# Performance work log

Hardware: AMD Instinct MI355X
Metric: run time of the kernel (lower is better)

Reference implementation:

```python
import jax, jax.numpy as jnp
import numpy as np

NEG_SLOPE = 0.2


def gat_layer(x, src, dst, W, a_src, a_dst, b, heads, out_c, concat):
    N = x.shape[0]
    h = (x @ W).reshape(N, heads, out_c)                      # [N,H,C]
    alpha_s = jnp.einsum('nhc,hc->nh', h, a_src)              # [N,H]
    alpha_d = jnp.einsum('nhc,hc->nh', h, a_dst)              # [N,H]
    e = jax.nn.leaky_relu(alpha_s[src] + alpha_d[dst], NEG_SLOPE)  # [E,H]
    # softmax over incoming edges per destination node (segment softmax)
    m = jax.ops.segment_max(e, dst, num_segments=N)
    m = jnp.where(jnp.isfinite(m), m, 0.0)
    ex = jnp.exp(e - m[dst])
    denom = jax.ops.segment_sum(ex, dst, num_segments=N)
    alpha = ex / (denom[dst] + 1e-16)                         # [E,H]
    out = jax.ops.segment_sum(alpha[:, :, None] * h[src], dst, num_segments=N)  # [N,H,C]
    out = out.reshape(N, heads * out_c) if concat else out.mean(axis=1)
    return out + b


def setup_inputs() -> dict:
    key = jax.random.key(0)
    ks = jax.random.split(key, 12)
    N, E, D, H, C, G = 20000, 160000, 256, 4, 128, 64
    x = jax.random.normal(ks[0], (N, D), dtype=jnp.float32)
    edge_index = jax.random.randint(ks[1], (2, E), 0, N)
    batch = jnp.sort(jax.random.randint(ks[2], (N,), 0, G))
    s = 0.05
    params = {
        'W1': jax.random.normal(ks[3], (D, H * C), jnp.float32) * s,
        'a_src1': jax.random.normal(ks[4], (H, C), jnp.float32) * s,
        'a_dst1': jax.random.normal(ks[5], (H, C), jnp.float32) * s,
        'b1': jnp.zeros((H * C,), jnp.float32),
        'W2': jax.random.normal(ks[6], (H * C, C), jnp.float32) * s,
        'a_src2': jax.random.normal(ks[7], (1, C), jnp.float32) * s,
        'a_dst2': jax.random.normal(ks[8], (1, C), jnp.float32) * s,
        'b2': jnp.zeros((C,), jnp.float32),
        'fc1_W': jax.random.normal(ks[9], (C, C // 2), jnp.float32) * s,
        'fc1_b': jnp.zeros((C // 2,), jnp.float32),
        'fc2_W': jax.random.normal(ks[10], (C // 2, 1), jnp.float32) * s,
        'fc2_b': jnp.zeros((1,), jnp.float32),
    }
    return dict(x=x, edge_index=edge_index, batch=batch, **params)


def reference(x, edge_index, batch, W1, a_src1, a_dst1, b1, W2, a_src2, a_dst2, b2,
              fc1_W, fc1_b, fc2_W, fc2_b):
    N = x.shape[0]
    G = 64  # number of graphs
    # add self-loops (PyG GATConv default)
    loop = jnp.arange(N, dtype=edge_index.dtype)
    src = jnp.concatenate([edge_index[0], loop])
    dst = jnp.concatenate([edge_index[1], loop])
    h = jax.nn.relu(gat_layer(x, src, dst, W1, a_src1, a_dst1, b1, 4, 128, True))
    h = gat_layer(h, src, dst, W2, a_src2, a_dst2, b2, 1, 128, False)
    # global mean pool per graph
    sums = jax.ops.segment_sum(h, batch, num_segments=G)
    cnts = jax.ops.segment_sum(jnp.ones((N,), h.dtype), batch, num_segments=G)
    pooled = sums / jnp.maximum(cnts, 1.0)[:, None]          # [G,128]
    out = jax.nn.relu(pooled @ fc1_W + fc1_b)
    return out @ fc2_W + fc2_b                                # [G,1]
```

## Files before the change

kernel.cpp:

```cpp
#include <hip/hip_runtime.h>
#include <hip/hip_bf16.h>
#include <cstdint>
#include <cstddef>

#define NEG_SLOPE 0.2f

typedef __attribute__((ext_vector_type(8))) __bf16 bf16x8;
typedef __attribute__((ext_vector_type(4))) __bf16 bf16x4;
typedef __attribute__((ext_vector_type(2))) __bf16 bf16x2;
typedef __attribute__((ext_vector_type(4))) float  f32x4;

template<int MF, int NF, bool STORE_BF16>
__global__ __launch_bounds__(256) void gemm_mfma(
    const __bf16* __restrict__ A, const __bf16* __restrict__ Bt,
    void* __restrict__ Cout, int M, int N, int K)
{
    const int tid  = threadIdx.x;
    const int wave = tid >> 6, lane = tid & 63;
    const int wr = wave >> 1, wc = wave & 1;
    const int rowbase = blockIdx.y * (32 * MF) + wr * (16 * MF);
    const int colbase = blockIdx.x * (32 * NF) + wc * (16 * NF);
    const int l15 = lane & 15, kg = lane >> 4;

    size_t aoff[MF], boff[NF];
    #pragma unroll
    for (int mf = 0; mf < MF; ++mf) {
        int r = rowbase + mf * 16 + l15;
        if (r > M - 1) r = M - 1;
        aoff[mf] = (size_t)r * K + kg * 8;
    }
    #pragma unroll
    for (int nf = 0; nf < NF; ++nf) {
        int c = colbase + nf * 16 + l15;
        boff[nf] = (size_t)c * K + kg * 8;
    }

    f32x4 acc[MF][NF];
    #pragma unroll
    for (int mf = 0; mf < MF; ++mf)
        #pragma unroll
        for (int nf = 0; nf < NF; ++nf)
            acc[mf][nf] = (f32x4){0.f, 0.f, 0.f, 0.f};

    #pragma unroll 2
    for (int k0 = 0; k0 < K; k0 += 32) {
        bf16x8 af[MF], bf[NF];
        #pragma unroll
        for (int mf = 0; mf < MF; ++mf)
            af[mf] = *(const bf16x8*)(A + aoff[mf] + k0);
        #pragma unroll
        for (int nf = 0; nf < NF; ++nf)
            bf[nf] = *(const bf16x8*)(Bt + boff[nf] + k0);
        #pragma unroll
        for (int mf = 0; mf < MF; ++mf)
            #pragma unroll
            for (int nf = 0; nf < NF; ++nf)
                acc[mf][nf] = __builtin_amdgcn_mfma_f32_16x16x32_bf16(af[mf], bf[nf], acc[mf][nf], 0, 0, 0);
    }

    #pragma unroll
    for (int mf = 0; mf < MF; ++mf)
        #pragma unroll
        for (int j = 0; j < 4; ++j) {
            int r = rowbase + mf * 16 + kg * 4 + j;
            if (r < M) {
                #pragma unroll
                for (int nf = 0; nf < NF; ++nf) {
                    int c = colbase + nf * 16 + l15;
                    if (STORE_BF16)
                        ((__bf16*)Cout)[(size_t)r * N + c] = (__bf16)acc[mf][nf][j];
                    else
                        ((float*)Cout)[(size_t)r * N + c] = acc[mf][nf][j];
                }
            }
        }
}

__global__ void prep_kernel(const float* __restrict__ W1, const float* __restrict__ W2,
                            const float* __restrict__ as1w, const float* __restrict__ ad1w,
                            const float* __restrict__ as2w, const float* __restrict__ ad2w,
                            const int* __restrict__ batch,
                            __bf16* __restrict__ w1t, __bf16* __restrict__ w2t,
                            float* __restrict__ wsd1, float* __restrict__ wsd2,
                            int* __restrict__ gstart, int* __restrict__ cnt,
                            int N, int G)
{
    int t = blockIdx.x * 256 + threadIdx.x;
    if (t < 131072) {
        int i = t;
        int k = i >> 9, n = i & 511;
        w1t[n * 256 + k] = (__bf16)W1[i];
    } else if (t < 196608) {
        int j = t - 131072;
        int k = j >> 7, n = j & 127;
        w2t[n * 512 + k] = (__bf16)W2[j];
    } else if (t < 199680) {
        int t2 = t - 196608;
        if (t2 < 2048) {
            int k = t2 >> 3, v = t2 & 7, h = v >> 1;
            const float* av = (v & 1) ? (ad1w + h * 128) : (as1w + h * 128);
            float s = 0.f;
            for (int c = 0; c < 128; ++c) s += W1[k * 512 + h * 128 + c] * av[c];
            wsd1[v * 256 + k] = s;
        } else {
            int t3 = t2 - 2048;
            int k = t3 >> 1, v = t3 & 1;
            const float* av = v ? ad2w : as2w;
            float s = 0.f;
            for (int c = 0; c < 128; ++c) s += W2[k * 128 + c] * av[c];
            wsd2[v * 512 + k] = s;
        }
    } else if (t < 199680 + N) {
        int n = t - 199680;
        int b    = batch[n];
        int prev = (n == 0) ? -1 : batch[n - 1];
        for (int g = prev + 1; g <= b; ++g) gstart[g] = n;
        if (n == N - 1) {
            for (int g = b + 1; g <= G; ++g) gstart[g] = N;
        }
    } else if (t < 199680 + 2 * N) {
        cnt[t - 199680 - N] = 0;
    }
}

__global__ __launch_bounds__(256) void cvtx_kernel(
    const float* __restrict__ x, const float* __restrict__ wsd1,
    __bf16* __restrict__ xb, float* __restrict__ as1_, float* __restrict__ ad1_, int N)
{
    int wave = threadIdx.x >> 6, lane = threadIdx.x & 63;
    int n = blockIdx.x * 4 + wave;
    if (n >= N) return;
    float4 xv = *(const float4*)&x[(size_t)n * 256 + lane * 4];
    bf16x4 xo;
    xo[0] = (__bf16)xv.x; xo[1] = (__bf16)xv.y; xo[2] = (__bf16)xv.z; xo[3] = (__bf16)xv.w;
    *(bf16x4*)&xb[(size_t)n * 256 + lane * 4] = xo;
    float p[8];
    #pragma unroll
    for (int v = 0; v < 8; ++v) {
        float4 wv = *(const float4*)&wsd1[v * 256 + lane * 4];
        p[v] = xv.x * wv.x + xv.y * wv.y + xv.z * wv.z + xv.w * wv.w;
    }
    #pragma unroll
    for (int v = 0; v < 8; ++v)
        #pragma unroll
        for (int s = 1; s < 64; s <<= 1) p[v] += __shfl_xor(p[v], s);
    if (lane == 0) {
        #pragma unroll
        for (int h = 0; h < 4; ++h) {
            as1_[n * 4 + h] = p[2 * h];
            ad1_[n * 4 + h] = p[2 * h + 1];
        }
    }
}

__global__ void count_kernel(const int* __restrict__ ei, int* __restrict__ cnt,
                             int ET, int E0)
{
    int e = blockIdx.x * blockDim.x + threadIdx.x;
    if (e >= ET) return;
    int d = (e < E0) ? ei[E0 + e] : (e - E0);
    atomicAdd(&cnt[d], 1);
}

__global__ __launch_bounds__(1024) void scan_fused(
    const int* __restrict__ cnt, int* __restrict__ offs, int* __restrict__ cur, int n)
{
    constexpr int CHUNK = 20;
    int t = threadIdx.x;
    int base = t * CHUNK;
    int v[CHUNK];
    int s = 0;
    #pragma unroll
    for (int i = 0; i < CHUNK; ++i) {
        int idx = base + i;
        int xv = (idx < n) ? cnt[idx] : 0;
        v[i] = s; s += xv;
    }
    int lane = t & 63, w = t >> 6;
    int sc = s;
    #pragma unroll
    for (int d = 1; d < 64; d <<= 1) {
        int o = __shfl_up(sc, d);
        if (lane >= d) sc += o;
    }
    __shared__ int wt[16], wb[17];
    if (lane == 63) wt[w] = sc;
    __syncthreads();
    if (t == 0) {
        int acc = 0;
        for (int i = 0; i < 16; ++i) { wb[i] = acc; acc += wt[i]; }
        wb[16] = acc;
    }
    __syncthreads();
    int ebase = wb[w] + (sc - s);
    #pragma unroll
    for (int i = 0; i < CHUNK; ++i) {
        int idx = base + i;
        if (idx < n) {
            int o = ebase + v[i];
            offs[idx] = o;
            cur[idx]  = o;
        }
    }
    if (t == 0) offs[n] = wb[16];
}

__global__ void scatter_kernel(const int* __restrict__ ei, int* __restrict__ cur,
                               int* __restrict__ eid, int ET, int E0)
{
    int e = blockIdx.x * blockDim.x + threadIdx.x;
    if (e >= ET) return;
    int d   = (e < E0) ? ei[E0 + e] : (e - E0);
    int pos = atomicAdd(&cur[d], 1);
    eid[pos] = e;
}

__global__ __launch_bounds__(256) void aggregate1_kernel(
    const __bf16* __restrict__ h1b, const int* __restrict__ offs,
    const int* __restrict__ eid, const int* __restrict__ ei,
    const float* __restrict__ as1_, const float* __restrict__ ad1_,
    const float* __restrict__ b1, const float* __restrict__ wsd2,
    __bf16* __restrict__ out1b, float* __restrict__ as2_, float* __restrict__ ad2_,
    int E0, int N)
{
    int wave = threadIdx.x >> 6, lane = threadIdx.x & 63;
    int n = blockIdx.x * 4 + wave;
    if (n >= N) return;
    int hd  = lane >> 4;
    int l16 = lane & 15;
    int s0 = offs[n], s1 = offs[n + 1];
    float adn = ad1_[n * 4 + hd];

    float m = -1e30f;
    for (int j = s0 + l16; j < s1; j += 16) {
        int e = eid[j];
        int s = (e < E0) ? ei[e] : (e - E0);
        float v = as1_[s * 4 + hd] + adn;
        v = (v < 0.f) ? NEG_SLOPE * v : v;
        m = fmaxf(m, v);
    }
    #pragma unroll
    for (int t = 1; t < 16; t <<= 1) m = fmaxf(m, __shfl_xor(m, t));

    float den = 0.f;
    float a[8] = {0.f, 0.f, 0.f, 0.f, 0.f, 0.f, 0.f, 0.f};
    const __bf16* hbase = h1b + lane * 8;
    int j = s0;
    for (; j + 7 < s1; j += 8) {
        int e_[8], s_[8];
        float v_[8];
        bf16x8 h_[8];
        #pragma unroll
        for (int i = 0; i < 8; ++i) e_[i] = eid[j + i];
        #pragma unroll
        for (int i = 0; i < 8; ++i) s_[i] = (e_[i] < E0) ? ei[e_[i]] : (e_[i] - E0);
        #pragma unroll
        for (int i = 0; i < 8; ++i) v_[i] = as1_[s_[i] * 4 + hd] + adn;
        #pragma unroll
        for (int i = 0; i < 8; ++i) h_[i] = *(const bf16x8*)(hbase + (size_t)s_[i] * 512);
        #pragma unroll
        for (int i = 0; i < 8; ++i) {
            float v = (v_[i] < 0.f) ? NEG_SLOPE * v_[i] : v_[i];
            float w = __expf(v - m);
            den += w;
            #pragma unroll
            for (int k = 0; k < 8; ++k)
                a[k] = fmaf(w, (float)h_[i][k], a[k]);
        }
    }
    for (; j < s1; ++j) {
        int e = eid[j];
        int s = (e < E0) ? ei[e] : (e - E0);
        float v = as1_[s * 4 + hd] + adn;
        v = (v < 0.f) ? NEG_SLOPE * v : v;
        float w = __expf(v - m);
        den += w;
        bf16x8 hv = *(const bf16x8*)(hbase + (size_t)s * 512);
        #pragma unroll
        for (int k = 0; k < 8; ++k) a[k] = fmaf(w, (float)hv[k], a[k]);
    }
    float inv = 1.f / (den + 1e-16f);

    bf16x8 ov;
    float ps = 0.f, pd = 0.f;
    #pragma unroll
    for (int i = 0; i < 8; ++i) {
        float o = fmaxf(a[i] * inv + b1[lane * 8 + i], 0.f);
        ov[i] = (__bf16)o;
        ps = fmaf(o, wsd2[lane * 8 + i], ps);
        pd = fmaf(o, wsd2[512 + lane * 8 + i], pd);
    }
    *(bf16x8*)&out1b[(size_t)n * 512 + lane * 8] = ov;
    #pragma unroll
    for (int t = 1; t < 64; t <<= 1) {
        ps += __shfl_xor(ps, t);
        pd += __shfl_xor(pd, t);
    }
    if (lane == 0) {
        as2_[n] = ps;
        ad2_[n] = pd;
    }
}

__global__ __launch_bounds__(256) void aggregate2_kernel(
    const __bf16* __restrict__ h2b, const int* __restrict__ offs,
    const int* __restrict__ eid, const int* __restrict__ ei,
    const float* __restrict__ as2_, const float* __restrict__ ad2_,
    const float* __restrict__ b2, float* __restrict__ out2, int E0, int N)
{
    int wave = threadIdx.x >> 6, lane = threadIdx.x & 63;
    int n = blockIdx.x * 4 + wave;
    if (n >= N) return;
    int s0 = offs[n], s1 = offs[n + 1];
    float adn = ad2_[n];

    float m = -1e30f;
    for (int j = s0 + lane; j < s1; j += 64) {
        int e = eid[j];
        int s = (e < E0) ? ei[e] : (e - E0);
        float v = as2_[s] + adn;
        v = (v < 0.f) ? NEG_SLOPE * v : v;
        m = fmaxf(m, v);
    }
    #pragma unroll
    for (int t = 1; t < 64; t <<= 1) m = fmaxf(m, __shfl_xor(m, t));

    float den = 0.f;
    float a0 = 0.f, a1 = 0.f;
    const __bf16* hbase = h2b + lane * 2;
    int j = s0;
    for (; j + 7 < s1; j += 8) {
        int e_[8], s_[8];
        float v_[8];
        bf16x2 h_[8];
        #pragma unroll
        for (int i = 0; i < 8; ++i) e_[i] = eid[j + i];
        #pragma unroll
        for (int i = 0; i < 8; ++i) s_[i] = (e_[i] < E0) ? ei[e_[i]] : (e_[i] - E0);
        #pragma unroll
        for (int i = 0; i < 8; ++i) v_[i] = as2_[s_[i]] + adn;
        #pragma unroll
        for (int i = 0; i < 8; ++i) h_[i] = *(const bf16x2*)(hbase + (size_t)s_[i] * 128);
        #pragma unroll
        for (int i = 0; i < 8; ++i) {
            float v = (v_[i] < 0.f) ? NEG_SLOPE * v_[i] : v_[i];
            float w = __expf(v - m);
            den += w;
            a0 = fmaf(w, (float)h_[i][0], a0);
            a1 = fmaf(w, (float)h_[i][1], a1);
        }
    }
    for (; j < s1; ++j) {
        int e = eid[j];
        int s = (e < E0) ? ei[e] : (e - E0);
        float v = as2_[s] + adn;
        v = (v < 0.f) ? NEG_SLOPE * v : v;
        float w = __expf(v - m);
        den += w;
        bf16x2 hv = *(const bf16x2*)(hbase + (size_t)s * 128);
        a0 = fmaf(w, (float)hv[0], a0);
        a1 = fmaf(w, (float)hv[1], a1);
    }
    float inv = 1.f / (den + 1e-16f);
    float2 o;
    o.x = a0 * inv + b2[lane * 2 + 0];
    o.y = a1 * inv + b2[lane * 2 + 1];
    *(float2*)&out2[(size_t)n * 128 + lane * 2] = o;
}

#define POOL_S 16
__global__ void pool_stage1(const float* __restrict__ out2, const int* __restrict__ gstart,
                            float* __restrict__ partial, int C)
{
    int g = blockIdx.x, slice = blockIdx.y;
    int c = threadIdx.x;
    int s = gstart[g], e = gstart[g + 1];
    int len = e - s;
    int chunk = (len + POOL_S - 1) / POOL_S;
    int n0 = s + slice * chunk;
    int n1 = min(n0 + chunk, e);
    float acc = 0.f;
    for (int n = n0; n < n1; ++n) acc += out2[(size_t)n * C + c];
    partial[((size_t)g * POOL_S + slice) * C + c] = acc;
}

__global__ __launch_bounds__(128) void pool_head(
    const float* __restrict__ partial, const int* __restrict__ gstart,
    const float* __restrict__ fc1W, const float* __restrict__ fc1b,
    const float* __restrict__ fc2W, const float* __restrict__ fc2b,
    float* __restrict__ out)
{
    int g = blockIdx.x;
    int t = threadIdx.x;
    __shared__ float pl[128];
    float acc = 0.f;
    #pragma unroll
    for (int s = 0; s < POOL_S; ++s)
        acc += partial[((size_t)g * POOL_S + s) * 128 + t];
    float cntf = (float)(gstart[g + 1] - gstart[g]);
    pl[t] = acc / fmaxf(cntf, 1.0f);
    __syncthreads();
    if (t < 64) {
        float v = 0.f;
        for (int c = 0; c < 128; ++c)
            v += pl[c] * fc1W[c * 64 + t];
        v = fmaxf(v + fc1b[t], 0.f) * fc2W[t];
        #pragma unroll
        for (int s = 32; s > 0; s >>= 1) v += __shfl_down(v, s);
        if (t == 0) out[g] = v + fc2b[0];
    }
}

extern "C" void kernel_launch(void* const* d_in, const int* in_sizes, int n_in,
                              void* d_out, int out_size, void* d_ws, size_t ws_size,
                              hipStream_t stream)
{
    const float* x    = (const float*)d_in[0];
    const int*   ei   = (const int*)d_in[1];
    const int*   batch= (const int*)d_in[2];
    const float* W1   = (const float*)d_in[3];
    const float* as1w = (const float*)d_in[4];
    const float* ad1w = (const float*)d_in[5];
    const float* b1   = (const float*)d_in[6];
    const float* W2   = (const float*)d_in[7];
    const float* as2w = (const float*)d_in[8];
    const float* ad2w = (const float*)d_in[9];
    const float* b2   = (const float*)d_in[10];
    const float* fc1W = (const float*)d_in[11];
    const float* fc1b = (const float*)d_in[12];
    const float* fc2W = (const float*)d_in[13];
    const float* fc2b = (const float*)d_in[14];
    float* out = (float*)d_out;

    const int D = 256, C = 128, HC = 512, G = 64;
    const int N  = in_sizes[0] / D;
    const int E0 = in_sizes[1] / 2;
    const int ET = E0 + N;

    char* p = (char*)d_ws;
    auto alloc = [&](size_t bytes) -> char* {
        char* r = p;
        p += (bytes + 255) & ~(size_t)255;
        return r;
    };
    __bf16* xb    = (__bf16*)alloc((size_t)N * D * 2);
    __bf16* h1b   = (__bf16*)alloc((size_t)N * HC * 2);
    __bf16* out1b = (__bf16*)alloc((size_t)N * HC * 2);
    __bf16* h2b   = (__bf16*)alloc((size_t)N * C * 2);
    float*  out2  = (float*)alloc((size_t)N * C * 4);
    __bf16* w1t   = (__bf16*)alloc((size_t)256 * 512 * 2);
    __bf16* w2t   = (__bf16*)alloc((size_t)512 * 128 * 2);
    float* wsd1 = (float*)alloc(8 * 256 * 4);
    float* wsd2 = (float*)alloc(2 * 512 * 4);
    float* as1_ = (float*)alloc((size_t)N * 4 * 4);
    float* ad1_ = (float*)alloc((size_t)N * 4 * 4);
    float* as2_ = (float*)alloc((size_t)N * 4);
    float* ad2_ = (float*)alloc((size_t)N * 4);
    int*   cnt    = (int*)alloc((size_t)N * 4);
    int*   cur    = (int*)alloc((size_t)N * 4);
    int*   offs   = (int*)alloc((size_t)(N + 1) * 4);
    int*   eid    = (int*)alloc((size_t)ET * 4);
    int*   gstart = (int*)alloc((size_t)(G + 1) * 4);
    float* partial= (float*)alloc((size_t)G * POOL_S * C * 4);

    {
        int total = 199680 + 2 * N;
        prep_kernel<<<(total + 255) / 256, 256, 0, stream>>>(
            W1, W2, as1w, ad1w, as2w, ad2w, batch,
            w1t, w2t, wsd1, wsd2, gstart, cnt, N, G);
    }

    count_kernel<<<(ET + 255) / 256, 256, 0, stream>>>(ei, cnt, ET, E0);
    scan_fused<<<1, 1024, 0, stream>>>(cnt, offs, cur, N);
    scatter_kernel<<<(ET + 255) / 256, 256, 0, stream>>>(ei, cur, eid, ET, E0);

    cvtx_kernel<<<N / 4, 256, 0, stream>>>(x, wsd1, xb, as1_, ad1_, N);

    gemm_mfma<4, 4, true><<<dim3(HC / 128, (N + 127) / 128), 256, 0, stream>>>(
        xb, w1t, h1b, N, HC, D);
    aggregate1_kernel<<<(N + 3) / 4, 256, 0, stream>>>(
        h1b, offs, eid, ei, as1_, ad1_, b1, wsd2, out1b, as2_, ad2_, E0, N);

    gemm_mfma<2, 2, true><<<dim3(C / 64, (N + 63) / 64), 256, 0, stream>>>(
        out1b, w2t, h2b, N, C, HC);
    aggregate2_kernel<<<(N + 3) / 4, 256, 0, stream>>>(
        h2b, offs, eid, ei, as2_, ad2_, b2, out2, E0, N);

    pool_stage1<<<dim3(G, POOL_S), C, 0, stream>>>(out2, gstart, partial, C);
    pool_head<<<G, 128, 0, stream>>>(partial, gstart, fc1W, fc1b, fc2W, fc2b, out);
}
```

Baseline: 196.7 us.

## Aggregate raw features before layer-1 GEMM and use a global-max softmax bound

Layer 1 now aggregates x (256-dim, per head) over incoming edges and only then multiplies by W1 per head, in a new fused GEMM that also applies bias, ReLU and the layer-2 attention projections. This works because the attention-weighted sum commutes with the linear map. The per-destination max pass is replaced by an upper bound, lrelu(global max of alpha_src + alpha_dst), computed once in the scan kernel, so one edge pass is removed. The trade-off is a larger aggregated buffer (N×1024 bf16) in place of h1, and a risk of exp underflow when the bound is loose. The count and cvtx kernels are merged and the two pooling kernels collapse into one, which cuts launches.

```diff
diff --git a/kernel.cpp b/kernel.cpp
--- a/kernel.cpp
+++ b/kernel.cpp
@@ -9,6 +9,10 @@
 typedef __attribute__((ext_vector_type(4))) __bf16 bf16x4;
 typedef __attribute__((ext_vector_type(2))) __bf16 bf16x2;
 typedef __attribute__((ext_vector_type(4))) float  f32x4;
+
+__device__ __forceinline__ float lrelu(float v) {
+    return (v < 0.f) ? NEG_SLOPE * v : v;
+}
 
 template<int MF, int NF, bool STORE_BF16>
 __global__ __launch_bounds__(256) void gemm_mfma(
@@ -44,18 +48,18 @@
 
     #pragma unroll 2
     for (int k0 = 0; k0 < K; k0 += 32) {
-        bf16x8 af[MF], bf[NF];
+        bf16x8 af[MF], bfr[NF];
         #pragma unroll
         for (int mf = 0; mf < MF; ++mf)
             af[mf] = *(const bf16x8*)(A + aoff[mf] + k0);
         #pragma unroll
         for (int nf = 0; nf < NF; ++nf)
-            bf[nf] = *(const bf16x8*)(Bt + boff[nf] + k0);
+            bfr[nf] = *(const bf16x8*)(Bt + boff[nf] + k0);
         #pragma unroll
         for (int mf = 0; mf < MF; ++mf)
             #pragma unroll
             for (int nf = 0; nf < NF; ++nf)
-                acc[mf][nf] = __builtin_amdgcn_mfma_f32_16x16x32_bf16(af[mf], bf[nf], acc[mf][nf], 0, 0, 0);
+                acc[mf][nf] = __builtin_amdgcn_mfma_f32_16x16x32_bf16(af[mf], bfr[nf], acc[mf][nf], 0, 0, 0);
     }
 
     #pragma unroll
@@ -74,6 +78,95 @@
                 }
             }
         }
+}
+
+__global__ __launch_bounds__(256) void gemm1_agg(
+    const __bf16* __restrict__ aggx,
+    const __bf16* __restrict__ w1t,
+    const float* __restrict__ b1, const float* __restrict__ wsd2,
+    __bf16* __restrict__ out1b,
+    float* __restrict__ ps_part, float* __restrict__ pd_part,
+    int M)
+{
+    const int head = blockIdx.x;
+    const int tid  = threadIdx.x;
+    const int wave = tid >> 6, lane = tid & 63;
+    const int wr = wave >> 1, wc = wave & 1;
+    const int rowbase = blockIdx.y * 128 + wr * 64;
+    const int l15 = lane & 15, kg = lane >> 4;
+
+    size_t aoff[4], boff[4];
+    #pragma unroll
+    for (int mf = 0; mf < 4; ++mf) {
+        int r = rowbase + mf * 16 + l15;
+        if (r > M - 1) r = M - 1;
+        aoff[mf] = (size_t)r * 1024 + head * 256 + kg * 8;
+    }
+    #pragma unroll
+    for (int nf = 0; nf < 4; ++nf) {
+        int c = head * 128 + wc * 64 + nf * 16 + l15;
+        boff[nf] = (size_t)c * 256 + kg * 8;
+    }
+
+    f32x4 acc[4][4];
+    #pragma unroll
+    for (int mf = 0; mf < 4; ++mf)
+        #pragma unroll
+        for (int nf = 0; nf < 4; ++nf)
+            acc[mf][nf] = (f32x4){0.f, 0.f, 0.f, 0.f};
+
+    #pragma unroll 2
+    for (int k0 = 0; k0 < 256; k0 += 32) {
+        bf16x8 af[4], bfr[4];
+        #pragma unroll
+        for (int mf = 0; mf < 4; ++mf)
+            af[mf] = *(const bf16x8*)(aggx + aoff[mf] + k0);
+        #pragma unroll
+        for (int nf = 0; nf < 4; ++nf)
+            bfr[nf] = *(const bf16x8*)(w1t + boff[nf] + k0);
+        #pragma unroll
+        for (int mf = 0; mf < 4; ++mf)
+            #pragma unroll
+            for (int nf = 0; nf < 4; ++nf)
+                acc[mf][nf] = __builtin_amdgcn_mfma_f32_16x16x32_bf16(af[mf], bfr[nf], acc[mf][nf], 0, 0, 0);
+    }
+
+    __shared__ float smp[2][128], smd[2][128];
+
+    #pragma unroll
+    for (int mf = 0; mf < 4; ++mf)
+        #pragma unroll
+        for (int j = 0; j < 4; ++j) {
+            int r = rowbase + mf * 16 + kg * 4 + j;
+            float ps = 0.f, pd = 0.f;
+            #pragma unroll
+            for (int nf = 0; nf < 4; ++nf) {
+                int col = head * 128 + wc * 64 + nf * 16 + l15;
+                float o = fmaxf(acc[mf][nf][j] + b1[col], 0.f);
+                if (r < M)
+                    out1b[(size_t)r * 512 + col] = (__bf16)o;
+                ps = fmaf(o, wsd2[col], ps);
+                pd = fmaf(o, wsd2[512 + col], pd);
+            }
+            #pragma unroll
+            for (int t = 1; t < 16; t <<= 1) {
+                ps += __shfl_xor(ps, t);
+                pd += __shfl_xor(pd, t);
+            }
+            if (l15 == 0) {
+                int lr = wr * 64 + mf * 16 + kg * 4 + j;
+                smp[wc][lr] = ps;
+                smd[wc][lr] = pd;
+            }
+        }
+    __syncthreads();
+    if (tid < 128) {
+        int r = blockIdx.y * 128 + tid;
+        if (r < M) {
+            ps_part[(size_t)r * 4 + head] = smp[0][tid] + smp[1][tid];
+            pd_part[(size_t)r * 4 + head] = smd[0][tid] + smd[1][tid];
+        }
+    }
 }
 
 __global__ void prep_kernel(const float* __restrict__ W1, const float* __restrict__ W2,
@@ -123,12 +216,22 @@
     }
 }
 
-__global__ __launch_bounds__(256) void cvtx_kernel(
+__global__ __launch_bounds__(256) void count_cvtx(
+    const int* __restrict__ ei, int* __restrict__ cnt,
     const float* __restrict__ x, const float* __restrict__ wsd1,
-    __bf16* __restrict__ xb, float* __restrict__ as1_, float* __restrict__ ad1_, int N)
-{
+    __bf16* __restrict__ xb, float* __restrict__ as1_, float* __restrict__ ad1_,
+    int ET, int E0, int N, int CB)
+{
+    if ((int)blockIdx.x < CB) {
+        int e = blockIdx.x * 256 + threadIdx.x;
+        if (e >= ET) return;
+        int d = (e < E0) ? ei[E0 + e] : (e - E0);
+        atomicAdd(&cnt[d], 1);
+        return;
+    }
+    int bid = blockIdx.x - CB;
     int wave = threadIdx.x >> 6, lane = threadIdx.x & 63;
-    int n = blockIdx.x * 4 + wave;
+    int n = bid * 4 + wave;
     if (n >= N) return;
     float4 xv = *(const float4*)&x[(size_t)n * 256 + lane * 4];
     bf16x4 xo;
@@ -153,17 +256,9 @@
     }
 }
 
-__global__ void count_kernel(const int* __restrict__ ei, int* __restrict__ cnt,
-                             int ET, int E0)
-{
-    int e = blockIdx.x * blockDim.x + threadIdx.x;
-    if (e >= ET) return;
-    int d = (e < E0) ? ei[E0 + e] : (e - E0);
-    atomicAdd(&cnt[d], 1);
-}
-
-__global__ __launch_bounds__(1024) void scan_fused(
-    const int* __restrict__ cnt, int* __restrict__ offs, int* __restrict__ cur, int n)
+__global__ __launch_bounds__(1024) void scan_gmax(
+    const int* __restrict__ cnt, int* __restrict__ offs, int* __restrict__ cur,
+    const float* __restrict__ as1_, float* __restrict__ gmax1, int n)
 {
     constexpr int CHUNK = 20;
     int t = threadIdx.x;
@@ -184,6 +279,7 @@
         if (lane >= d) sc += o;
     }
     __shared__ int wt[16], wb[17];
+    __shared__ float gsm[16][4];
     if (lane == 63) wt[w] = sc;
     __syncthreads();
     if (t == 0) {
@@ -203,6 +299,32 @@
         }
     }
     if (t == 0) offs[n] = wb[16];
+
+    float lm0 = -1e30f, lm1 = -1e30f, lm2 = -1e30f, lm3 = -1e30f;
+    for (int i = t; i < n; i += 1024) {
+        float4 a = *(const float4*)&as1_[(size_t)i * 4];
+        lm0 = fmaxf(lm0, a.x); lm1 = fmaxf(lm1, a.y);
+        lm2 = fmaxf(lm2, a.z); lm3 = fmaxf(lm3, a.w);
+    }
+    #pragma unroll
+    for (int d = 1; d < 64; d <<= 1) {
+        lm0 = fmaxf(lm0, __shfl_xor(lm0, d));
+        lm1 = fmaxf(lm1, __shfl_xor(lm1, d));
+        lm2 = fmaxf(lm2, __shfl_xor(lm2, d));
+        lm3 = fmaxf(lm3, __shfl_xor(lm3, d));
+    }
+    if (lane == 0) {
+        gsm[w][0] = lm0; gsm[w][1] = lm1; gsm[w][2] = lm2; gsm[w][3] = lm3;
+    }
+    __syncthreads();
+    if (t == 0) {
+        float m0 = -1e30f, m1 = -1e30f, m2 = -1e30f, m3 = -1e30f;
+        for (int i = 0; i < 16; ++i) {
+            m0 = fmaxf(m0, gsm[i][0]); m1 = fmaxf(m1, gsm[i][1]);
+            m2 = fmaxf(m2, gsm[i][2]); m3 = fmaxf(m3, gsm[i][3]);
+        }
+        gmax1[0] = m0; gmax1[1] = m1; gmax1[2] = m2; gmax1[3] = m3;
+    }
 }
 
 __global__ void scatter_kernel(const int* __restrict__ ei, int* __restrict__ cur,
@@ -215,198 +337,191 @@
     eid[pos] = e;
 }
 
-__global__ __launch_bounds__(256) void aggregate1_kernel(
-    const __bf16* __restrict__ h1b, const int* __restrict__ offs,
+__global__ __launch_bounds__(256) void aggx_kernel(
+    const __bf16* __restrict__ xb, const int* __restrict__ offs,
     const int* __restrict__ eid, const int* __restrict__ ei,
     const float* __restrict__ as1_, const float* __restrict__ ad1_,
-    const float* __restrict__ b1, const float* __restrict__ wsd2,
-    __bf16* __restrict__ out1b, float* __restrict__ as2_, float* __restrict__ ad2_,
-    int E0, int N)
-{
-    int wave = threadIdx.x >> 6, lane = threadIdx.x & 63;
-    int n = blockIdx.x * 4 + wave;
-    if (n >= N) return;
-    int hd  = lane >> 4;
-    int l16 = lane & 15;
-    int s0 = offs[n], s1 = offs[n + 1];
-    float adn = ad1_[n * 4 + hd];
-
-    float m = -1e30f;
-    for (int j = s0 + l16; j < s1; j += 16) {
-        int e = eid[j];
-        int s = (e < E0) ? ei[e] : (e - E0);
-        float v = as1_[s * 4 + hd] + adn;
-        v = (v < 0.f) ? NEG_SLOPE * v : v;
-        m = fmaxf(m, v);
-    }
-    #pragma unroll
-    for (int t = 1; t < 16; t <<= 1) m = fmaxf(m, __shfl_xor(m, t));
-
-    float den = 0.f;
-    float a[8] = {0.f, 0.f, 0.f, 0.f, 0.f, 0.f, 0.f, 0.f};
-    const __bf16* hbase = h1b + lane * 8;
-    int j = s0;
-    for (; j + 7 < s1; j += 8) {
-        int e_[8], s_[8];
-        float v_[8];
-        bf16x8 h_[8];
-        #pragma unroll
-        for (int i = 0; i < 8; ++i) e_[i] = eid[j + i];
-        #pragma unroll
-        for (int i = 0; i < 8; ++i) s_[i] = (e_[i] < E0) ? ei[e_[i]] : (e_[i] - E0);
-        #pragma unroll
-        for (int i = 0; i < 8; ++i) v_[i] = as1_[s_[i] * 4 + hd] + adn;
-        #pragma unroll
-        for (int i = 0; i < 8; ++i) h_[i] = *(const bf16x8*)(hbase + (size_t)s_[i] * 512);
-        #pragma unroll
-        for (int i = 0; i < 8; ++i) {
-            float v = (v_[i] < 0.f) ? NEG_SLOPE * v_[i] : v_[i];
-            float w = __expf(v - m);
-            den += w;
-            #pragma unroll
-            for (int k = 0; k < 8; ++k)
-                a[k] = fmaf(w, (float)h_[i][k], a[k]);
-        }
-    }
-    for (; j < s1; ++j) {
-        int e = eid[j];
-        int s = (e < E0) ? ei[e] : (e - E0);
-        float v = as1_[s * 4 + hd] + adn;
-        v = (v < 0.f) ? NEG_SLOPE * v : v;
-        float w = __expf(v - m);
-        den += w;
-        bf16x8 hv = *(const bf16x8*)(hbase + (size_t)s * 512);
-        #pragma unroll
-        for (int k = 0; k < 8; ++k) a[k] = fmaf(w, (float)hv[k], a[k]);
-    }
-    float inv = 1.f / (den + 1e-16f);
-
-    bf16x8 ov;
-    float ps = 0.f, pd = 0.f;
-    #pragma unroll
-    for (int i = 0; i < 8; ++i) {
-        float o = fmaxf(a[i] * inv + b1[lane * 8 + i], 0.f);
-        ov[i] = (__bf16)o;
-        ps = fmaf(o, wsd2[lane * 8 + i], ps);
-        pd = fmaf(o, wsd2[512 + lane * 8 + i], pd);
-    }
-    *(bf16x8*)&out1b[(size_t)n * 512 + lane * 8] = ov;
-    #pragma unroll
-    for (int t = 1; t < 64; t <<= 1) {
-        ps += __shfl_xor(ps, t);
-        pd += __shfl_xor(pd, t);
-    }
-    if (lane == 0) {
-        as2_[n] = ps;
-        ad2_[n] = pd;
-    }
-}
-
-__global__ __launch_bounds__(256) void aggregate2_kernel(
-    const __bf16* __restrict__ h2b, const int* __restrict__ offs,
-    const int* __restrict__ eid, const int* __restrict__ ei,
-    const float* __restrict__ as2_, const float* __restrict__ ad2_,
-    const float* __restrict__ b2, float* __restrict__ out2, int E0, int N)
+    const float* __restrict__ gmax1,
+    __bf16* __restrict__ aggx, int E0, int N)
 {
     int wave = threadIdx.x >> 6, lane = threadIdx.x & 63;
     int n = blockIdx.x * 4 + wave;
     if (n >= N) return;
     int s0 = offs[n], s1 = offs[n + 1];
-    float adn = ad2_[n];
+    float4 adv = *(const float4*)&ad1_[(size_t)n * 4];
+    float m0 = lrelu(gmax1[0] + adv.x);
+    float m1 = lrelu(gmax1[1] + adv.y);
+    float m2 = lrelu(gmax1[2] + adv.z);
+    float m3 = lrelu(gmax1[3] + adv.w);
+
+    float d0 = 0.f, d1 = 0.f, d2 = 0.f, d3 = 0.f;
+    float a0[4] = {0.f,0.f,0.f,0.f}, a1[4] = {0.f,0.f,0.f,0.f};
+    float a2[4] = {0.f,0.f,0.f,0.f}, a3[4] = {0.f,0.f,0.f,0.f};
+    const __bf16* xbase = xb + lane * 4;
+
+    int j = s0;
+    for (; j + 7 < s1; j += 8) {
+        int s_[8]; float4 av_[8]; bf16x4 xv_[8];
+        #pragma unroll
+        for (int i = 0; i < 8; ++i) {
+            int e = eid[j + i];
+            s_[i] = (e < E0) ? ei[e] : (e - E0);
+        }
+        #pragma unroll
+        for (int i = 0; i < 8; ++i) av_[i] = *(const float4*)&as1_[(size_t)s_[i] * 4];
+        #pragma unroll
+        for (int i = 0; i < 8; ++i) xv_[i] = *(const bf16x4*)(xbase + (size_t)s_[i] * 256);
+        #pragma unroll
+        for (int i = 0; i < 8; ++i) {
+            float w0 = __expf(lrelu(av_[i].x + adv.x) - m0); d0 += w0;
+            float w1 = __expf(lrelu(av_[i].y + adv.y) - m1); d1 += w1;
+            float w2 = __expf(lrelu(av_[i].z + adv.z) - m2); d2 += w2;
+            float w3 = __expf(lrelu(av_[i].w + adv.w) - m3); d3 += w3;
+            float xf[4];
+            #pragma unroll
+            for (int c = 0; c < 4; ++c) xf[c] = (float)xv_[i][c];
+            #pragma unroll
+            for (int c = 0; c < 4; ++c) {
+                a0[c] = fmaf(w0, xf[c], a0[c]);
+                a1[c] = fmaf(w1, xf[c], a1[c]);
+                a2[c] = fmaf(w2, xf[c], a2[c]);
+                a3[c] = fmaf(w3, xf[c], a3[c]);
+            }
+        }
+    }
+    for (; j < s1; ++j) {
+        int e = eid[j];
+        int s = (e < E0) ? ei[e] : (e - E0);
+        float4 av = *(const float4*)&as1_[(size_t)s * 4];
+        bf16x4 xv = *(const bf16x4*)(xbase + (size_t)s * 256);
+        float w0 = __expf(lrelu(av.x + adv.x) - m0); d0 += w0;
+        float w1 = __expf(lrelu(av.y + adv.y) - m1); d1 += w1;
+        float w2 = __expf(lrelu(av.z + adv.z) - m2); d2 += w2;
+        float w3 = __expf(lrelu(av.w + adv.w) - m3); d3 += w3;
+        float xf[4];
+        #pragma unroll
+        for (int c = 0; c < 4; ++c) xf[c] = (float)xv[c];
+        #pragma unroll
+        for (int c = 0; c < 4; ++c) {
+            a0[c] = fmaf(w0, xf[c], a0[c]);
+            a1[c] = fmaf(w1, xf[c], a1[c]);
+            a2[c] = fmaf(w2, xf[c], a2[c]);
+            a3[c] = fmaf(w3, xf[c], a3[c]);
+        }
+    }
+
+    float i0 = 1.f / (d0 + 1e-16f);
+    float i1 = 1.f / (d1 + 1e-16f);
+    float i2 = 1.f / (d2 + 1e-16f);
+    float i3 = 1.f / (d3 + 1e-16f);
+    __bf16* obase = aggx + (size_t)n * 1024 + lane * 4;
+    bf16x4 o;
+    #pragma unroll
+    for (int c = 0; c < 4; ++c) o[c] = (__bf16)(a0[c] * i0);
+    *(bf16x4*)(obase + 0)   = o;
+    #pragma unroll
+    for (int c = 0; c < 4; ++c) o[c] = (__bf16)(a1[c] * i1);
+    *(bf16x4*)(obase + 256) = o;
+    #pragma unroll
+    for (int c = 0; c < 4; ++c) o[c] = (__bf16)(a2[c] * i2);
+    *(bf16x4*)(obase + 512) = o;
+    #pragma unroll
+    for (int c = 0; c < 4; ++c) o[c] = (__bf16)(a3[c] * i3);
+    *(bf16x4*)(obase + 768) = o;
+}
+
+__global__ __launch_bounds__(256) void aggregate2_kernel(
+    const __bf16* __restrict__ h2b, const int* __restrict__ offs,
+    const int* __restrict__ eid, const int* __restrict__ ei,
+    const float* __restrict__ ps_part, const float* __restrict__ pd_part,
+    const float* __restrict__ b2, float* __restrict__ out2, int E0, int N)
+{
+    int wave = threadIdx.x >> 6, lane = threadIdx.x & 63;
+    int n = blockIdx.x * 4 + wave;
+    if (n >= N) return;
+    int s0 = offs[n], s1 = offs[n + 1];
+    float4 pdv = *(const float4*)&pd_part[(size_t)n * 4];
+    float adn = (pdv.x + pdv.y) + (pdv.z + pdv.w);
 
     float m = -1e30f;
     for (int j = s0 + lane; j < s1; j += 64) {
         int e = eid[j];
         int s = (e < E0) ? ei[e] : (e - E0);
-        float v = as2_[s] + adn;
-        v = (v < 0.f) ? NEG_SLOPE * v : v;
+        float4 pv = *(const float4*)&ps_part[(size_t)s * 4];
+        float v = lrelu(((pv.x + pv.y) + (pv.z + pv.w)) + adn);
         m = fmaxf(m, v);
     }
     #pragma unroll
     for (int t = 1; t < 64; t <<= 1) m = fmaxf(m, __shfl_xor(m, t));
 
     float den = 0.f;
-    float a0 = 0.f, a1 = 0.f;
+    float c0 = 0.f, c1 = 0.f;
     const __bf16* hbase = h2b + lane * 2;
     int j = s0;
     for (; j + 7 < s1; j += 8) {
-        int e_[8], s_[8];
-        float v_[8];
-        bf16x2 h_[8];
-        #pragma unroll
-        for (int i = 0; i < 8; ++i) e_[i] = eid[j + i];
-        #pragma unroll
-        for (int i = 0; i < 8; ++i) s_[i] = (e_[i] < E0) ? ei[e_[i]] : (e_[i] - E0);
-        #pragma unroll
-        for (int i = 0; i < 8; ++i) v_[i] = as2_[s_[i]] + adn;
+        int s_[8]; float4 pv_[8]; bf16x2 h_[8];
+        #pragma unroll
+        for (int i = 0; i < 8; ++i) {
+            int e = eid[j + i];
+            s_[i] = (e < E0) ? ei[e] : (e - E0);
+        }
+        #pragma unroll
+        for (int i = 0; i < 8; ++i) pv_[i] = *(const float4*)&ps_part[(size_t)s_[i] * 4];
         #pragma unroll
         for (int i = 0; i < 8; ++i) h_[i] = *(const bf16x2*)(hbase + (size_t)s_[i] * 128);
         #pragma unroll
         for (int i = 0; i < 8; ++i) {
-            float v = (v_[i] < 0.f) ? NEG_SLOPE * v_[i] : v_[i];
+            float v = lrelu(((pv_[i].x + pv_[i].y) + (pv_[i].z + pv_[i].w)) + adn);
             float w = __expf(v - m);
             den += w;
-            a0 = fmaf(w, (float)h_[i][0], a0);
-            a1 = fmaf(w, (float)h_[i][1], a1);
+            c0 = fmaf(w, (float)h_[i][0], c0);
+            c1 = fmaf(w, (float)h_[i][1], c1);
         }
     }
     for (; j < s1; ++j) {
         int e = eid[j];
         int s = (e < E0) ? ei[e] : (e - E0);
-        float v = as2_[s] + adn;
-        v = (v < 0.f) ? NEG_SLOPE * v : v;
+        float4 pv = *(const float4*)&ps_part[(size_t)s * 4];
+        float v = lrelu(((pv.x + pv.y) + (pv.z + pv.w)) + adn);
         float w = __expf(v - m);
         den += w;
         bf16x2 hv = *(const bf16x2*)(hbase + (size_t)s * 128);
-        a0 = fmaf(w, (float)hv[0], a0);
-        a1 = fmaf(w, (float)hv[1], a1);
+        c0 = fmaf(w, (float)hv[0], c0);
+        c1 = fmaf(w, (float)hv[1], c1);
     }
     float inv = 1.f / (den + 1e-16f);
     float2 o;
-    o.x = a0 * inv + b2[lane * 2 + 0];
-    o.y = a1 * inv + b2[lane * 2 + 1];
+    o.x = c0 * inv + b2[lane * 2 + 0];
+    o.y = c1 * inv + b2[lane * 2 + 1];
     *(float2*)&out2[(size_t)n * 128 + lane * 2] = o;
 }
 
-#define POOL_S 16
-__global__ void pool_stage1(const float* __restrict__ out2, const int* __restrict__ gstart,
-                            float* __restrict__ partial, int C)
-{
-    int g = blockIdx.x, slice = blockIdx.y;
-    int c = threadIdx.x;
-    int s = gstart[g], e = gstart[g + 1];
-    int len = e - s;
-    int chunk = (len + POOL_S - 1) / POOL_S;
-    int n0 = s + slice * chunk;
-    int n1 = min(n0 + chunk, e);
-    float acc = 0.f;
-    for (int n = n0; n < n1; ++n) acc += out2[(size_t)n * C + c];
-    partial[((size_t)g * POOL_S + slice) * C + c] = acc;
-}
-
-__global__ __launch_bounds__(128) void pool_head(
-    const float* __restrict__ partial, const int* __restrict__ gstart,
+__global__ __launch_bounds__(256) void pool_head(
+    const float* __restrict__ out2, const int* __restrict__ gstart,
     const float* __restrict__ fc1W, const float* __restrict__ fc1b,
     const float* __restrict__ fc2W, const float* __restrict__ fc2b,
     float* __restrict__ out)
 {
     int g = blockIdx.x;
     int t = threadIdx.x;
-    __shared__ float pl[128];
+    int s = gstart[g], e = gstart[g + 1];
+    int c = t & 127, half = t >> 7;
     float acc = 0.f;
-    #pragma unroll
-    for (int s = 0; s < POOL_S; ++s)
-        acc += partial[((size_t)g * POOL_S + s) * 128 + t];
-    float cntf = (float)(gstart[g + 1] - gstart[g]);
-    pl[t] = acc / fmaxf(cntf, 1.0f);
+    for (int n = s + half; n < e; n += 2)
+        acc += out2[(size_t)n * 128 + c];
+    __shared__ float sm[2][128];
+    sm[half][c] = acc;
+    __syncthreads();
+    if (t < 128)
+        sm[0][t] = (sm[0][t] + sm[1][t]) / fmaxf((float)(e - s), 1.0f);
     __syncthreads();
     if (t < 64) {
         float v = 0.f;
-        for (int c = 0; c < 128; ++c)
-            v += pl[c] * fc1W[c * 64 + t];
+        for (int cc = 0; cc < 128; ++cc)
+            v += sm[0][cc] * fc1W[cc * 64 + t];
         v = fmaxf(v + fc1b[t], 0.f) * fc2W[t];
         #pragma unroll
-        for (int s = 32; s > 0; s >>= 1) v += __shfl_down(v, s);
+        for (int d = 32; d > 0; d >>= 1) v += __shfl_down(v, d);
         if (t == 0) out[g] = v + fc2b[0];
     }
 }
@@ -432,7 +547,7 @@
     const float* fc2b = (const float*)d_in[14];
     float* out = (float*)d_out;
 
-    const int D = 256, C = 128, HC = 512, G = 64;
+    const int D = 256, C = 128, G = 64;
     const int N  = in_sizes[0] / D;
     const int E0 = in_sizes[1] / 2;
     const int ET = E0 + N;
@@ -444,24 +559,24 @@
         return r;
     };
     __bf16* xb    = (__bf16*)alloc((size_t)N * D * 2);
-    __bf16* h1b   = (__bf16*)alloc((size_t)N * HC * 2);
-    __bf16* out1b = (__bf16*)alloc((size_t)N * HC * 2);
+    __bf16* aggx  = (__bf16*)alloc((size_t)N * 4 * 256 * 2);
+    __bf16* out1b = (__bf16*)alloc((size_t)N * 512 * 2);
     __bf16* h2b   = (__bf16*)alloc((size_t)N * C * 2);
     float*  out2  = (float*)alloc((size_t)N * C * 4);
     __bf16* w1t   = (__bf16*)alloc((size_t)256 * 512 * 2);
     __bf16* w2t   = (__bf16*)alloc((size_t)512 * 128 * 2);
-    float* wsd1 = (float*)alloc(8 * 256 * 4);
-    float* wsd2 = (float*)alloc(2 * 512 * 4);
-    float* as1_ = (float*)alloc((size_t)N * 4 * 4);
-    float* ad1_ = (float*)alloc((size_t)N * 4 * 4);
-    float* as2_ = (float*)alloc((size_t)N * 4);
-    float* ad2_ = (float*)alloc((size_t)N * 4);
+    float* wsd1   = (float*)alloc(8 * 256 * 4);
+    float* wsd2   = (float*)alloc(2 * 512 * 4);
+    float* gmax1  = (float*)alloc(4 * 4);
+    float* as1_   = (float*)alloc((size_t)N * 4 * 4);
+    float* ad1_   = (float*)alloc((size_t)N * 4 * 4);
+    float* ps_part= (float*)alloc((size_t)N * 4 * 4);
+    float* pd_part= (float*)alloc((size_t)N * 4 * 4);
     int*   cnt    = (int*)alloc((size_t)N * 4);
     int*   cur    = (int*)alloc((size_t)N * 4);
     int*   offs   = (int*)alloc((size_t)(N + 1) * 4);
     int*   eid    = (int*)alloc((size_t)ET * 4);
     int*   gstart = (int*)alloc((size_t)(G + 1) * 4);
-    float* partial= (float*)alloc((size_t)G * POOL_S * C * 4);
 
     {
         int total = 199680 + 2 * N;
@@ -470,22 +585,27 @@
             w1t, w2t, wsd1, wsd2, gstart, cnt, N, G);
     }
 
-    count_kernel<<<(ET + 255) / 256, 256, 0, stream>>>(ei, cnt, ET, E0);
-    scan_fused<<<1, 1024, 0, stream>>>(cnt, offs, cur, N);
+    {
+        int CB = (ET + 255) / 256;
+        count_cvtx<<<CB + N / 4, 256, 0, stream>>>(
+            ei, cnt, x, wsd1, xb, as1_, ad1_, ET, E0, N, CB);
+    }
+
+    scan_gmax<<<1, 1024, 0, stream>>>(cnt, offs, cur, as1_, gmax1, N);
+
     scatter_kernel<<<(ET + 255) / 256, 256, 0, stream>>>(ei, cur, eid, ET, E0);
 
-    cvtx_kernel<<<N / 4, 256, 0, stream>>>(x, wsd1, xb, as1_, ad1_, N);
-
-    gemm_mfma<4, 4, true><<<dim3(HC / 128, (N + 127) / 128), 256, 0, stream>>>(
-        xb, w1t, h1b, N, HC, D);
-    aggregate1_kernel<<<(N + 3) / 4, 256, 0, stream>>>(
-        h1b, offs, eid, ei, as1_, ad1_, b1, wsd2, out1b, as2_, ad2_, E0, N);
+    aggx_kernel<<<(N + 3) / 4, 256, 0, stream>>>(
+        xb, offs, eid, ei, as1_, ad1_, gmax1, aggx, E0, N);
+
+    gemm1_agg<<<dim3(4, (N + 127) / 128), 256, 0, stream>>>(
+        aggx, w1t, b1, wsd2, out1b, ps_part, pd_part, N);
 
     gemm_mfma<2, 2, true><<<dim3(C / 64, (N + 63) / 64), 256, 0, stream>>>(
-        out1b, w2t, h2b, N, C, HC);
+        out1b, w2t, h2b, N, C, 512);
+
     aggregate2_kernel<<<(N + 3) / 4, 256, 0, stream>>>(
-        h2b, offs, eid, ei, as2_, ad2_, b2, out2, E0, N);
-
-    pool_stage1<<<dim3(G, POOL_S), C, 0, stream>>>(out2, gstart, partial, C);
-    pool_head<<<G, 128, 0, stream>>>(partial, gstart, fc1W, fc1b, fc2W, fc2b, out);
-}
+        h2b, offs, eid, ei, ps_part, pd_part, b2, out2, E0, N);
+
+    pool_head<<<G, 256, 0, stream>>>(out2, gstart, fc1W, fc1b, fc2W, fc2b, out);
+}
```

Result: slower. 254.2 us (+29.2%).
